# Performance work log

Measured on AMD Instinct MI355X. Metric: run time of the kernel, lower is better.

## Reference

```python
import jax, jax.numpy as jnp
import numpy as np

B, S, H, F, E, K = 2, 2048, 1024, 4096, 8, 2


def setup_inputs() -> dict:
    key = jax.random.key(0)
    ks = jax.random.split(key, 6)
    x = jax.random.normal(ks[0], (B, S, H), dtype=jnp.float32)
    probs = jax.random.uniform(ks[1], (K, B, S, 1), dtype=jnp.float32)
    experts = jax.random.randint(ks[2], (K, B, S, 1), 0, E, dtype=jnp.int32)
    # per-expert FFN params; 0.02 scale mimics typical transformer init
    w1 = jax.random.normal(ks[3], (E, H, F), dtype=jnp.float32) * 0.02
    b1 = jnp.zeros((E, F), dtype=jnp.float32)
    w2 = jax.random.normal(ks[4], (E, F, H), dtype=jnp.float32) * 0.02
    b2 = jnp.zeros((E, H), dtype=jnp.float32)
    return {"x": x, "probs": probs, "experts": experts,
            "w1": w1, "b1": b1, "w2": w2, "b2": b2}


def reference(x, probs, experts, w1, b1, w2, b2):
    # Dense compute-all-experts FFN: every expert processes every token.
    h = jnp.einsum('bsh,ehf->ebsf', x, w1) + b1[:, None, None, :]  # [E,B,S,F]
    h = jax.nn.gelu(h)
    y = jnp.einsum('ebsf,efh->ebsh', h, w2) + b2[:, None, None, :]  # [E,B,S,H]
    # Masked combine: sum_e sum_j probs_j * y_e * (experts_j == e)
    onehot = jax.nn.one_hot(experts[..., 0], w1.shape[0], dtype=x.dtype)  # [K,B,S,E]
    weights = jnp.einsum('kbsl,kbse->bse', probs, onehot)  # [B,S,E]
    out = jnp.einsum('bse,ebsh->bsh', weights, y)
    return out
```

## Files before the change

kernel.cpp:

```cpp
#include <hip/hip_runtime.h>
#include <stdint.h>

#define H_DIM 1024
#define F_DIM 4096
#define E_NUM 8
#define T_NUM 4096
#define NE    8192
#define BM    256
#define BN    256
#define BK    64
#define MAXT  40
#define PADM  9984
#define TBY   65536
#define LDSSZ (2*TBY)

#define G1_NWG (MAXT * (F_DIM / BN))
#define TRW2_NWG 4096

#define M_NT  0
#define M_PB  1
#define M_CNT 16
#define M_CUR 24
#define M_TE  32
#define M_TR  72
#define M_INTS 112

typedef float  f32x4  __attribute__((ext_vector_type(4)));
typedef short  bf16x8 __attribute__((ext_vector_type(8)));
typedef __bf16 b16v8  __attribute__((ext_vector_type(8)));
typedef unsigned short u16;
typedef u16    u16x8  __attribute__((ext_vector_type(8)));

#define BAR() __builtin_amdgcn_s_barrier()

__device__ __forceinline__ float gelu_tanh(float v) {
  float u = 0.7978845608028654f * (v + 0.044715f * v * v * v);
  return v / (1.0f + __expf(-2.0f * u));
}

__device__ __forceinline__ float b2f(u16 v) {
  union { float f; unsigned u; } x; x.u = ((unsigned)v) << 16; return x.f;
}

__device__ __forceinline__ void gl16(const void* g, void* l) {
  __builtin_amdgcn_global_load_lds(
      (const __attribute__((address_space(1))) unsigned int*)g,
      (__attribute__((address_space(3))) unsigned int*)l, 16, 0, 0);
}

__device__ __forceinline__ void trans_tile(const float* __restrict__ W, u16* __restrict__ Wt,
                                           int R, int C, int e, int bx, int by,
                                           char* L, int tid) {
  int r0 = by * 64, c0 = bx * 64;
  const float* We = W + (size_t)e * R * C;
  u16* Wte = Wt + (size_t)e * R * C;
#pragma unroll
  for (int it = 0; it < 4; ++it) {
    int gi = it * 256 + tid;
    int row = gi >> 4, c4 = gi & 15;
    f32x4 v = *(const f32x4*)(We + (size_t)(r0 + row) * C + c0 + c4 * 4);
    *(f32x4*)(L + row * 256 + ((c4 ^ (row & 15)) * 16)) = v;
  }
  __syncthreads();
#pragma unroll
  for (int s = 0; s < 2; ++s) {
    int chunk = s * 256 + tid;
    int c = chunk >> 3, rb = chunk & 7;
    b16v8 o;
#pragma unroll
    for (int j = 0; j < 8; ++j) {
      int r = rb * 8 + j;
      float f = *(const float*)(L + r * 256 + (((c >> 2) ^ (r & 15)) * 16) + (c & 3) * 4);
      o[j] = (__bf16)f;
    }
    *(b16v8*)(void*)(Wte + (size_t)(c0 + c) * R + r0 + rb * 8) = o;
  }
}


__global__ void k_init(int* tok, float* wgt, int* meta) {
  int i = blockIdx.x * 256 + threadIdx.x;
  if (i < PADM) { tok[i] = 0; wgt[i] = 0.f; }
  if (i < E_NUM) { meta[M_CNT + i] = 0; meta[M_CUR + i] = 0; }
}

__global__ void k_count(const int* __restrict__ experts, int* meta) {
  int i = blockIdx.x * 256 + threadIdx.x;
  int e = experts[i];
  int lane = threadIdx.x & 63;
#pragma unroll
  for (int ee = 0; ee < E_NUM; ++ee) {
    unsigned long long bm = __ballot(e == ee);
    if (e == ee && lane == __builtin_ctzll(bm))
      atomicAdd(&meta[M_CNT + ee], __popcll(bm));
  }
}

__global__ void k_plan(int* meta) {
  if (threadIdx.x != 0 || blockIdx.x != 0) return;
  int pb = 0, idx = 0;
  for (int e = 0; e < E_NUM; ++e) {
    int c = meta[M_CNT + e];
    int nt = (c + BM - 1) / BM;
    meta[M_PB + e] = pb;
    for (int t = 0; t < nt && idx < MAXT; ++t) {
      meta[M_TE + idx] = e; meta[M_TR + idx] = pb + t * BM; ++idx;
    }
    pb += nt * BM;
  }
  meta[M_NT] = idx;
}

__global__ void k_scatter(const int* __restrict__ experts, const float* __restrict__ probs,
                          int* tok, float* wgt, int* entpos, int* meta) {
  int i = blockIdx.x * 256 + threadIdx.x;
  int e = experts[i];
  int t = i & (T_NUM - 1);
  float p = probs[i];
  int lane = threadIdx.x & 63;
#pragma unroll
  for (int ee = 0; ee < E_NUM; ++ee) {
    unsigned long long bm = __ballot(e == ee);
    if (e == ee) {
      int leader = __builtin_ctzll(bm);
      int cnt = __popcll(bm);
      int base = 0;
      if (lane == leader) base = atomicAdd(&meta[M_CUR + ee], cnt);
      base = __shfl(base, leader);
      int rank = __popcll(bm & ((1ull << lane) - 1ull));
      int pos = meta[M_PB + ee] + base + rank;
      tok[pos] = t;
      wgt[pos] = p;
      entpos[i] = pos;
    }
  }
}

#define TRW1_NWG 4096
__global__ __launch_bounds__(512) void k_prep(const float* __restrict__ x, u16* __restrict__ xbf,
                                              const float* __restrict__ w1, u16* __restrict__ w1t) {
  int bid = blockIdx.x;
  if (bid < TRW1_NWG) {
    alignas(16) __shared__ char L[32768];
    int ti = bid * 2 + (threadIdx.x >> 8);
    int e = ti >> 10, rem = ti & 1023;
    int bx = rem & 63, by = rem >> 6;
    trans_tile(w1, w1t, H_DIM, F_DIM, e, bx, by, L + (threadIdx.x >> 8) * 16384, threadIdx.x & 255);
    return;
  }
  int i = (bid - TRW1_NWG) * 512 + threadIdx.x;
  const f32x4* xp = (const f32x4*)x;
  f32x4 a = xp[i * 2], b = xp[i * 2 + 1];
  b16v8 o;
  o[0] = (__bf16)a[0]; o[1] = (__bf16)a[1]; o[2] = (__bf16)a[2]; o[3] = (__bf16)a[3];
  o[4] = (__bf16)b[0]; o[5] = (__bf16)b[1]; o[6] = (__bf16)b[2]; o[7] = (__bf16)b[3];
  ((b16v8*)xbf)[i] = o;
}

__global__ __launch_bounds__(256) void k_trans(const float* __restrict__ W, u16* __restrict__ Wt,
                                               int R, int C) {
  alignas(16) __shared__ char L[16384];
  trans_tile(W, Wt, R, C, blockIdx.z, blockIdx.x, blockIdx.y, L, threadIdx.x);
}


#define STAGEALL(kt, sb)                                                      \
  { _Pragma("unroll")                                                         \
    for (int j = 0; j < 4; ++j)                                               \
      gl16(asrc[j] + (size_t)(kt) * BK, LDS + (sb) + j * 8192 + wid * 1024);  \
    _Pragma("unroll")                                                         \
    for (int j = 0; j < 4; ++j)                                               \
      gl16(bsrc[j] + (size_t)(kt) * BK, LDS + (sb) + 32768 + j * 8192 + wid * 1024); }

#define GEMM_COMPUTE(bb)                                                      \
  { const char* Ab_ = LDS + (bb); const char* Bb_ = LDS + (bb) + 32768;       \
    _Pragma("unroll")                                                         \
    for (int kk = 0; kk < 2; ++kk) {                                          \
      int kbyte = kk * 64 + ((lane >> 4) << 4);                               \
      bf16x8 af[8], bfr[4];                                                   \
      _Pragma("unroll")                                                       \
      for (int m = 0; m < 8; ++m) {                                           \
        int r = wr * 128 + m * 16 + (lane & 15);                              \
        af[m] = *(const bf16x8*)(Ab_ + r * 128 + (kbyte ^ ((r & 7) << 4)));   \
      }                                                                       \
      _Pragma("unroll")                                                       \
      for (int n = 0; n < 4; ++n) {                                           \
        int c = wc * 64 + n * 16 + (lane & 15);                               \
        bfr[n] = *(const bf16x8*)(Bb_ + c * 128 + (kbyte ^ ((c & 7) << 4)));  \
      }                                                                       \
      __builtin_amdgcn_s_setprio(1);                                          \
      _Pragma("unroll")                                                       \
      for (int m = 0; m < 8; ++m)                                             \
        _Pragma("unroll")                                                     \
        for (int n = 0; n < 4; ++n)                                           \
          acc[m][n] = __builtin_amdgcn_mfma_f32_16x16x32_bf16(af[m], bfr[n], acc[m][n], 0, 0, 0); \
      __builtin_amdgcn_s_setprio(0);                                          \
    } }

#define GEMM_KLOOP(NT)                                                        \
  STAGEALL(0, 0);                                                             \
  asm volatile("s_waitcnt vmcnt(0)" ::: "memory");                            \
  BAR();                                                                      \
  { int cur = 0;                                                              \
    for (int kt = 0; kt < (NT); ++kt) {                                       \
      if (kt + 1 < (NT)) STAGEALL(kt + 1, (cur ^ 1) * TBY);                   \
      GEMM_COMPUTE(cur * TBY);                                                \
      asm volatile("s_waitcnt vmcnt(0)" ::: "memory");                        \
      BAR();                                                                  \
      cur ^= 1;                                                               \
    } }


__global__ __launch_bounds__(512, 1) void k_gemm1(
    const u16* __restrict__ xbf, const u16* __restrict__ w1t, const float* __restrict__ b1,
    const int* __restrict__ tok, const int* __restrict__ meta, u16* __restrict__ hbuf,
    const float* __restrict__ w2, u16* __restrict__ w2t)
{
  extern __shared__ char LDS[];
  int wg = blockIdx.x;
  if (wg >= G1_NWG) {
    int ti = (wg - G1_NWG) * 2 + (threadIdx.x >> 8);
    int e = ti >> 10, rem = ti & 1023;
    int bx = rem & 15, by = rem >> 4;
    trans_tile(w2, w2t, F_DIM, H_DIM, e, bx, by, LDS + (threadIdx.x >> 8) * 16384, threadIdx.x & 255);
    return;
  }
  int work = (wg & 7) * (G1_NWG / 8) + (wg >> 3);
  int slot = work % MAXT;
  int cbase = (work / MAXT) * BN;
  int nt = meta[M_NT];
  if (slot >= nt) return;
  int e     = meta[M_TE + slot];
  int rbase = meta[M_TR + slot];

  int tid = threadIdx.x;
  int lane = tid & 63;
  int wid = tid >> 6;
  int wr = wid >> 2, wc = wid & 3;
  int cc = tid & 7, rr = tid >> 3;

  const u16* asrc[4]; const u16* bsrc[4];
#pragma unroll
  for (int j = 0; j < 4; ++j) {
    int rj = j * 64 + rr;
    int t = tok[rbase + rj];
    asrc[j] = xbf + (size_t)t * H_DIM + ((cc ^ (rj & 7)) * 8);
    bsrc[j] = w1t + ((size_t)e * F_DIM + cbase + rj) * H_DIM + ((cc ^ (rj & 7)) * 8);
  }

  f32x4 acc[8][4];
#pragma unroll
  for (int m = 0; m < 8; ++m)
#pragma unroll
    for (int n = 0; n < 4; ++n) acc[m][n] = (f32x4){0.f, 0.f, 0.f, 0.f};

  GEMM_KLOOP(H_DIM / BK)

  float bv[4];
#pragma unroll
  for (int n = 0; n < 4; ++n) bv[n] = b1[e * F_DIM + cbase + wc * 64 + n * 16 + (lane & 15)];
  char* reg = LDS + wid * 16384;
#pragma unroll
  for (int m = 0; m < 8; ++m)
#pragma unroll
    for (int n = 0; n < 4; ++n)
#pragma unroll
      for (int q = 0; q < 4; ++q) {
        float v = acc[m][n][q] + bv[n];
        v = gelu_tanh(v);
        int row4 = ((lane >> 4) << 2) + q;
        int col = n * 16 + (lane & 15);
        *(__bf16*)(reg + m * 2048 + row4 * 128 + col * 2) = (__bf16)v;
      }
#pragma unroll
  for (int q = 0; q < 16; ++q) {
    int m = q >> 1, p = q & 1;
    int byte = p * 1024 + lane * 16;
    u16x8 v = *(const u16x8*)(reg + m * 2048 + byte);
    int row  = p * 8 + (lane >> 3);
    int colb = (lane & 7) * 16;
    size_t grow = (size_t)(rbase + wr * 128 + m * 16 + row);
    size_t gcol = (size_t)(cbase + wc * 64 + (colb >> 1));
    *(u16x8*)(hbuf + grow * F_DIM + gcol) = v;
  }
}


__global__ __launch_bounds__(512, 1) void k_gemm2(
    const u16* __restrict__ hbuf, const u16* __restrict__ w2t, const float* __restrict__ b2,
    const int* __restrict__ meta, u16* __restrict__ ybuf)
{
  extern __shared__ char LDS[];
  int wg = blockIdx.x;
  int work = (wg & 7) * 40 + (wg >> 3);
  int zi   = work / 160;
  int rem  = work % 160;
  int slot = rem % MAXT;
  int cbase = (rem / MAXT) * BN;
  int kzb   = zi * (F_DIM / 2);
  int nt = meta[M_NT];
  if (slot >= nt) return;
  int e     = meta[M_TE + slot];
  int rbase = meta[M_TR + slot];

  int tid = threadIdx.x;
  int lane = tid & 63;
  int wid = tid >> 6;
  int wr = wid >> 2, wc = wid & 3;
  int cc = tid & 7, rr = tid >> 3;

  const u16* asrc[4]; const u16* bsrc[4];
#pragma unroll
  for (int j = 0; j < 4; ++j) {
    int rj = j * 64 + rr;
    asrc[j] = hbuf + (size_t)(rbase + rj) * F_DIM + kzb + ((cc ^ (rj & 7)) * 8);
    bsrc[j] = w2t + ((size_t)e * H_DIM + cbase + rj) * F_DIM + kzb + ((cc ^ (rj & 7)) * 8);
  }

  f32x4 acc[8][4];
#pragma unroll
  for (int m = 0; m < 8; ++m)
#pragma unroll
    for (int n = 0; n < 4; ++n) acc[m][n] = (f32x4){0.f, 0.f, 0.f, 0.f};

  GEMM_KLOOP((F_DIM / 2) / BK)

  bool z0 = (zi == 0);
  u16* yb = ybuf + (size_t)zi * PADM * H_DIM;
  float bv[4];
#pragma unroll
  for (int n = 0; n < 4; ++n)
    bv[n] = z0 ? b2[e * H_DIM + cbase + wc * 64 + n * 16 + (lane & 15)] : 0.f;
  char* reg = LDS + wid * 16384;
#pragma unroll
  for (int m = 0; m < 8; ++m)
#pragma unroll
    for (int n = 0; n < 4; ++n)
#pragma unroll
      for (int q = 0; q < 4; ++q) {
        float v = acc[m][n][q] + bv[n];
        int row4 = ((lane >> 4) << 2) + q;
        int col = n * 16 + (lane & 15);
        *(__bf16*)(reg + m * 2048 + row4 * 128 + col * 2) = (__bf16)v;
      }
#pragma unroll
  for (int q = 0; q < 16; ++q) {
    int m = q >> 1, p = q & 1;
    int byte = p * 1024 + lane * 16;
    u16x8 v = *(const u16x8*)(reg + m * 2048 + byte);
    int row  = p * 8 + (lane >> 3);
    int colb = (lane & 7) * 16;
    size_t grow = (size_t)(rbase + wr * 128 + m * 16 + row);
    size_t gcol = (size_t)(cbase + wc * 64 + (colb >> 1));
    *(u16x8*)(yb + grow * H_DIM + gcol) = v;
  }
}


__global__ __launch_bounds__(256) void k_combine(
    const u16* __restrict__ ybuf, const float* __restrict__ wgt,
    const int* __restrict__ entpos, float* __restrict__ out)
{
  int idx = blockIdx.x * 256 + threadIdx.x;
  int t = idx >> 7, hc = idx & 127;
  int p0 = entpos[t], p1 = entpos[T_NUM + t];
  float w0 = wgt[p0], w1 = wgt[p1];
  const u16x8* y0 = (const u16x8*)(ybuf);
  const u16x8* y1 = (const u16x8*)(ybuf + (size_t)PADM * H_DIM);
  u16x8 a = y0[(size_t)p0 * (H_DIM / 8) + hc];
  u16x8 b = y1[(size_t)p0 * (H_DIM / 8) + hc];
  u16x8 c = y0[(size_t)p1 * (H_DIM / 8) + hc];
  u16x8 d = y1[(size_t)p1 * (H_DIM / 8) + hc];
  f32x4 o0, o1;
#pragma unroll
  for (int j = 0; j < 4; ++j)
    o0[j] = w0 * (b2f(a[j]) + b2f(b[j])) + w1 * (b2f(c[j]) + b2f(d[j]));
#pragma unroll
  for (int j = 0; j < 4; ++j)
    o1[j] = w0 * (b2f(a[4 + j]) + b2f(b[4 + j])) + w1 * (b2f(c[4 + j]) + b2f(d[4 + j]));
  f32x4* op = (f32x4*)(out + (size_t)t * H_DIM + hc * 8);
  op[0] = o0;
  op[1] = o1;
}


extern "C" void kernel_launch(void* const* d_in, const int* in_sizes, int n_in,
                              void* d_out, int out_size, void* d_ws, size_t ws_size,
                              hipStream_t stream)
{
  const float* x       = (const float*)d_in[0];
  const float* probs   = (const float*)d_in[1];
  const int*   experts = (const int*)d_in[2];
  const float* w1      = (const float*)d_in[3];
  const float* b1      = (const float*)d_in[4];
  const float* w2      = (const float*)d_in[5];
  const float* b2      = (const float*)d_in[6];
  float* out = (float*)d_out;

  char* ws = (char*)d_ws;
  size_t off = 0;
  u16*   hbuf = (u16*)(ws + off);  off += (size_t)PADM * F_DIM * sizeof(u16);
  u16*   xbf  = (u16*)(ws + off);  off += (size_t)T_NUM * H_DIM * sizeof(u16);
  u16*   w1t  = (u16*)(ws + off);  off += (size_t)E_NUM * F_DIM * H_DIM * sizeof(u16);
  u16*   ybuf = (u16*)(ws + off);  off += (size_t)2 * PADM * H_DIM * sizeof(u16);
  int*   tok  = (int*)(ws + off);  off += (size_t)PADM * sizeof(int);
  float* wgt  = (float*)(ws + off); off += (size_t)PADM * sizeof(float);
  int*   entpos = (int*)(ws + off); off += (size_t)NE * sizeof(int);
  int*   meta = (int*)(ws + off);  off += M_INTS * sizeof(int);
  size_t w2t_bytes = (size_t)E_NUM * F_DIM * H_DIM * sizeof(u16);
  bool fused = (ws_size >= off + w2t_bytes);
  u16* w2t = fused ? (u16*)(ws + off) : w1t;
  (void)in_sizes; (void)n_in;

  hipFuncSetAttribute(reinterpret_cast<const void*>(&k_gemm1),
                      hipFuncAttributeMaxDynamicSharedMemorySize, LDSSZ);
  hipFuncSetAttribute(reinterpret_cast<const void*>(&k_gemm2),
                      hipFuncAttributeMaxDynamicSharedMemorySize, LDSSZ);

  k_init   <<<dim3((PADM + 255) / 256), 256, 0, stream>>>(tok, wgt, meta);
  k_count  <<<dim3(NE / 256), 256, 0, stream>>>(experts, meta);
  k_plan   <<<1, 1, 0, stream>>>(meta);
  k_scatter<<<dim3(NE / 256), 256, 0, stream>>>(experts, probs, tok, wgt, entpos, meta);
  k_prep   <<<dim3(TRW1_NWG + T_NUM * H_DIM / 8 / 512), 512, 0, stream>>>(x, xbf, w1, w1t);
  k_gemm1  <<<dim3(G1_NWG + (fused ? TRW2_NWG : 0)), 512, LDSSZ, stream>>>(
              xbf, w1t, b1, tok, meta, hbuf, w2, w2t);
  if (!fused)
    k_trans<<<dim3(H_DIM / 64, F_DIM / 64, E_NUM), 256, 0, stream>>>(w2, w2t, F_DIM, H_DIM);
  k_gemm2  <<<dim3(MAXT * (H_DIM / BN) * 2), 512, LDSSZ, stream>>>(hbuf, w2t, b2, meta, ybuf);
  k_combine<<<dim3(T_NUM * H_DIM / 8 / 256), 256, 0, stream>>>(ybuf, wgt, entpos, out);
}
```

Baseline: 341.4 us.

## Use persistent grid-stride GEMM2 with four-way split-K reusing w1t workspace

```diff
diff --git a/kernel.cpp b/kernel.cpp
--- a/kernel.cpp
+++ b/kernel.cpp
@@ -16,6 +16,7 @@
 
 #define G1_NWG (MAXT * (F_DIM / BN))
 #define TRW2_NWG 4096
+#define TRW1_NWG 4096
 
 #define M_NT  0
 #define M_PB  1
@@ -136,7 +137,6 @@
   }
 }
 
-#define TRW1_NWG 4096
 __global__ __launch_bounds__(512) void k_prep(const float* __restrict__ x, u16* __restrict__ xbf,
                                               const float* __restrict__ w1, u16* __restrict__ w1t) {
   int bid = blockIdx.x;
@@ -286,22 +286,17 @@
 }
 
 
+template<int ZS, int GRID>
 __global__ __launch_bounds__(512, 1) void k_gemm2(
     const u16* __restrict__ hbuf, const u16* __restrict__ w2t, const float* __restrict__ b2,
     const int* __restrict__ meta, u16* __restrict__ ybuf)
 {
   extern __shared__ char LDS[];
+  const int NIT = MAXT * 4 * ZS;
+  const int KT  = (F_DIM / ZS) / BK;
   int wg = blockIdx.x;
-  int work = (wg & 7) * 40 + (wg >> 3);
-  int zi   = work / 160;
-  int rem  = work % 160;
-  int slot = rem % MAXT;
-  int cbase = (rem / MAXT) * BN;
-  int kzb   = zi * (F_DIM / 2);
+  int work0 = (wg & 7) * (GRID / 8) + (wg >> 3);
   int nt = meta[M_NT];
-  if (slot >= nt) return;
-  int e     = meta[M_TE + slot];
-  int rbase = meta[M_TR + slot];
 
   int tid = threadIdx.x;
   int lane = tid & 63;
@@ -309,54 +304,69 @@
   int wr = wid >> 2, wc = wid & 3;
   int cc = tid & 7, rr = tid >> 3;
 
-  const u16* asrc[4]; const u16* bsrc[4];
-#pragma unroll
-  for (int j = 0; j < 4; ++j) {
-    int rj = j * 64 + rr;
-    asrc[j] = hbuf + (size_t)(rbase + rj) * F_DIM + kzb + ((cc ^ (rj & 7)) * 8);
-    bsrc[j] = w2t + ((size_t)e * H_DIM + cbase + rj) * F_DIM + kzb + ((cc ^ (rj & 7)) * 8);
-  }
-
-  f32x4 acc[8][4];
-#pragma unroll
-  for (int m = 0; m < 8; ++m)
-#pragma unroll
-    for (int n = 0; n < 4; ++n) acc[m][n] = (f32x4){0.f, 0.f, 0.f, 0.f};
-
-  GEMM_KLOOP((F_DIM / 2) / BK)
-
-  bool z0 = (zi == 0);
-  u16* yb = ybuf + (size_t)zi * PADM * H_DIM;
-  float bv[4];
-#pragma unroll
-  for (int n = 0; n < 4; ++n)
-    bv[n] = z0 ? b2[e * H_DIM + cbase + wc * 64 + n * 16 + (lane & 15)] : 0.f;
-  char* reg = LDS + wid * 16384;
-#pragma unroll
-  for (int m = 0; m < 8; ++m)
+  for (int item = work0; item < NIT; item += GRID) {
+    int slot = item / (4 * ZS);
+    int rem  = item % (4 * ZS);
+    int cb   = rem / ZS;
+    int zi   = rem % ZS;
+    if (slot >= nt) continue;
+    int e     = meta[M_TE + slot];
+    int rbase = meta[M_TR + slot];
+    int cbase = cb * BN;
+    int kzb   = zi * (F_DIM / ZS);
+
+    __syncthreads();
+
+    const u16* asrc[4]; const u16* bsrc[4];
+#pragma unroll
+    for (int j = 0; j < 4; ++j) {
+      int rj = j * 64 + rr;
+      asrc[j] = hbuf + (size_t)(rbase + rj) * F_DIM + kzb + ((cc ^ (rj & 7)) * 8);
+      bsrc[j] = w2t + ((size_t)e * H_DIM + cbase + rj) * F_DIM + kzb + ((cc ^ (rj & 7)) * 8);
+    }
+
+    f32x4 acc[8][4];
+#pragma unroll
+    for (int m = 0; m < 8; ++m)
+#pragma unroll
+      for (int n = 0; n < 4; ++n) acc[m][n] = (f32x4){0.f, 0.f, 0.f, 0.f};
+
+    GEMM_KLOOP(KT)
+
+    bool z0 = (zi == 0);
+    u16* yb = ybuf + (size_t)zi * PADM * H_DIM;
+    float bv[4];
 #pragma unroll
     for (int n = 0; n < 4; ++n)
-#pragma unroll
-      for (int q = 0; q < 4; ++q) {
-        float v = acc[m][n][q] + bv[n];
-        int row4 = ((lane >> 4) << 2) + q;
-        int col = n * 16 + (lane & 15);
-        *(__bf16*)(reg + m * 2048 + row4 * 128 + col * 2) = (__bf16)v;
-      }
-#pragma unroll
-  for (int q = 0; q < 16; ++q) {
-    int m = q >> 1, p = q & 1;
-    int byte = p * 1024 + lane * 16;
-    u16x8 v = *(const u16x8*)(reg + m * 2048 + byte);
-    int row  = p * 8 + (lane >> 3);
-    int colb = (lane & 7) * 16;
-    size_t grow = (size_t)(rbase + wr * 128 + m * 16 + row);
-    size_t gcol = (size_t)(cbase + wc * 64 + (colb >> 1));
-    *(u16x8*)(yb + grow * H_DIM + gcol) = v;
-  }
-}
-
-
+      bv[n] = z0 ? b2[e * H_DIM + cbase + wc * 64 + n * 16 + (lane & 15)] : 0.f;
+    char* reg = LDS + wid * 16384;
+#pragma unroll
+    for (int m = 0; m < 8; ++m)
+#pragma unroll
+      for (int n = 0; n < 4; ++n)
+#pragma unroll
+        for (int q = 0; q < 4; ++q) {
+          float v = acc[m][n][q] + bv[n];
+          int row4 = ((lane >> 4) << 2) + q;
+          int col = n * 16 + (lane & 15);
+          *(__bf16*)(reg + m * 2048 + row4 * 128 + col * 2) = (__bf16)v;
+        }
+#pragma unroll
+    for (int q = 0; q < 16; ++q) {
+      int m = q >> 1, p = q & 1;
+      int byte = p * 1024 + lane * 16;
+      u16x8 v = *(const u16x8*)(reg + m * 2048 + byte);
+      int row  = p * 8 + (lane >> 3);
+      int colb = (lane & 7) * 16;
+      size_t grow = (size_t)(rbase + wr * 128 + m * 16 + row);
+      size_t gcol = (size_t)(cbase + wc * 64 + (colb >> 1));
+      *(u16x8*)(yb + grow * H_DIM + gcol) = v;
+    }
+  }
+}
+
+
+template<int ZS>
 __global__ __launch_bounds__(256) void k_combine(
     const u16* __restrict__ ybuf, const float* __restrict__ wgt,
     const int* __restrict__ entpos, float* __restrict__ out)
@@ -365,19 +375,22 @@
   int t = idx >> 7, hc = idx & 127;
   int p0 = entpos[t], p1 = entpos[T_NUM + t];
   float w0 = wgt[p0], w1 = wgt[p1];
-  const u16x8* y0 = (const u16x8*)(ybuf);
-  const u16x8* y1 = (const u16x8*)(ybuf + (size_t)PADM * H_DIM);
-  u16x8 a = y0[(size_t)p0 * (H_DIM / 8) + hc];
-  u16x8 b = y1[(size_t)p0 * (H_DIM / 8) + hc];
-  u16x8 c = y0[(size_t)p1 * (H_DIM / 8) + hc];
-  u16x8 d = y1[(size_t)p1 * (H_DIM / 8) + hc];
+  float s0[8], s1[8];
+#pragma unroll
+  for (int j = 0; j < 8; ++j) { s0[j] = 0.f; s1[j] = 0.f; }
+#pragma unroll
+  for (int z = 0; z < ZS; ++z) {
+    const u16x8* yz = (const u16x8*)(ybuf + (size_t)z * PADM * H_DIM);
+    u16x8 a = yz[(size_t)p0 * (H_DIM / 8) + hc];
+    u16x8 b = yz[(size_t)p1 * (H_DIM / 8) + hc];
+#pragma unroll
+    for (int j = 0; j < 8; ++j) { s0[j] += b2f(a[j]); s1[j] += b2f(b[j]); }
+  }
   f32x4 o0, o1;
 #pragma unroll
-  for (int j = 0; j < 4; ++j)
-    o0[j] = w0 * (b2f(a[j]) + b2f(b[j])) + w1 * (b2f(c[j]) + b2f(d[j]));
-#pragma unroll
-  for (int j = 0; j < 4; ++j)
-    o1[j] = w0 * (b2f(a[4 + j]) + b2f(b[4 + j])) + w1 * (b2f(c[4 + j]) + b2f(d[4 + j]));
+  for (int j = 0; j < 4; ++j) o0[j] = w0 * s0[j] + w1 * s1[j];
+#pragma unroll
+  for (int j = 0; j < 4; ++j) o1[j] = w0 * s0[4 + j] + w1 * s1[4 + j];
   f32x4* op = (f32x4*)(out + (size_t)t * H_DIM + hc * 8);
   op[0] = o0;
   op[1] = o1;
@@ -410,11 +423,14 @@
   size_t w2t_bytes = (size_t)E_NUM * F_DIM * H_DIM * sizeof(u16);
   bool fused = (ws_size >= off + w2t_bytes);
   u16* w2t = fused ? (u16*)(ws + off) : w1t;
+  u16* ybuf4 = w1t;
   (void)in_sizes; (void)n_in;
 
   hipFuncSetAttribute(reinterpret_cast<const void*>(&k_gemm1),
                       hipFuncAttributeMaxDynamicSharedMemorySize, LDSSZ);
-  hipFuncSetAttribute(reinterpret_cast<const void*>(&k_gemm2),
+  hipFuncSetAttribute(reinterpret_cast<const void*>(&k_gemm2<4, 512>),
+                      hipFuncAttributeMaxDynamicSharedMemorySize, LDSSZ);
+  hipFuncSetAttribute(reinterpret_cast<const void*>(&k_gemm2<2, 320>),
                       hipFuncAttributeMaxDynamicSharedMemorySize, LDSSZ);
 
   k_init   <<<dim3((PADM + 255) / 256), 256, 0, stream>>>(tok, wgt, meta);
@@ -424,8 +440,12 @@
   k_prep   <<<dim3(TRW1_NWG + T_NUM * H_DIM / 8 / 512), 512, 0, stream>>>(x, xbf, w1, w1t);
   k_gemm1  <<<dim3(G1_NWG + (fused ? TRW2_NWG : 0)), 512, LDSSZ, stream>>>(
               xbf, w1t, b1, tok, meta, hbuf, w2, w2t);
-  if (!fused)
+  if (fused) {
+    k_gemm2<4, 512><<<dim3(512), 512, LDSSZ, stream>>>(hbuf, w2t, b2, meta, ybuf4);
+    k_combine<4><<<dim3(T_NUM * H_DIM / 8 / 256), 256, 0, stream>>>(ybuf4, wgt, entpos, out);
+  } else {
     k_trans<<<dim3(H_DIM / 64, F_DIM / 64, E_NUM), 256, 0, stream>>>(w2, w2t, F_DIM, H_DIM);
-  k_gemm2  <<<dim3(MAXT * (H_DIM / BN) * 2), 512, LDSSZ, stream>>>(hbuf, w2t, b2, meta, ybuf);
-  k_combine<<<dim3(T_NUM * H_DIM / 8 / 256), 256, 0, stream>>>(ybuf, wgt, entpos, out);
-}
+    k_gemm2<2, 320><<<dim3(320), 512, LDSSZ, stream>>>(hbuf, w2t, b2, meta, ybuf);
+    k_combine<2><<<dim3(T_NUM * H_DIM / 8 / 256), 256, 0, stream>>>(ybuf, wgt, entpos, out);
+  }
+}
```

New measurement: 369.8 us. +8.3%, slower.

## Restructure GEMM k-loop into 8-phase schedule interleaving LDS reads, global stages, MFMAs

Applied to the files above, without the earlier changes.

```diff
diff --git a/kernel.cpp b/kernel.cpp
--- a/kernel.cpp
+++ b/kernel.cpp
@@ -16,6 +16,7 @@
 
 #define G1_NWG (MAXT * (F_DIM / BN))
 #define TRW2_NWG 4096
+#define TRW1_NWG 4096
 
 #define M_NT  0
 #define M_PB  1
@@ -31,7 +32,9 @@
 typedef unsigned short u16;
 typedef u16    u16x8  __attribute__((ext_vector_type(8)));
 
-#define BAR() __builtin_amdgcn_s_barrier()
+#define BAR()   __builtin_amdgcn_s_barrier()
+#define FENCE() asm volatile("" ::: "memory")
+#define LGKM0() asm volatile("s_waitcnt lgkmcnt(0)" ::: "memory")
 
 __device__ __forceinline__ float gelu_tanh(float v) {
   float u = 0.7978845608028654f * (v + 0.044715f * v * v * v);
@@ -136,7 +139,6 @@
   }
 }
 
-#define TRW1_NWG 4096
 __global__ __launch_bounds__(512) void k_prep(const float* __restrict__ x, u16* __restrict__ xbf,
                                               const float* __restrict__ w1, u16* __restrict__ w1t) {
   int bid = blockIdx.x;
@@ -164,48 +166,70 @@
 }
 
 
-#define STAGEALL(kt, sb)                                                      \
-  { _Pragma("unroll")                                                         \
-    for (int j = 0; j < 4; ++j)                                               \
-      gl16(asrc[j] + (size_t)(kt) * BK, LDS + (sb) + j * 8192 + wid * 1024);  \
-    _Pragma("unroll")                                                         \
-    for (int j = 0; j < 4; ++j)                                               \
-      gl16(bsrc[j] + (size_t)(kt) * BK, LDS + (sb) + 32768 + j * 8192 + wid * 1024); }
-
-#define GEMM_COMPUTE(bb)                                                      \
-  { const char* Ab_ = LDS + (bb); const char* Bb_ = LDS + (bb) + 32768;       \
-    _Pragma("unroll")                                                         \
-    for (int kk = 0; kk < 2; ++kk) {                                          \
-      int kbyte = kk * 64 + ((lane >> 4) << 4);                               \
-      bf16x8 af[8], bfr[4];                                                   \
-      _Pragma("unroll")                                                       \
-      for (int m = 0; m < 8; ++m) {                                           \
-        int r = wr * 128 + m * 16 + (lane & 15);                              \
-        af[m] = *(const bf16x8*)(Ab_ + r * 128 + (kbyte ^ ((r & 7) << 4)));   \
-      }                                                                       \
-      _Pragma("unroll")                                                       \
-      for (int n = 0; n < 4; ++n) {                                           \
-        int c = wc * 64 + n * 16 + (lane & 15);                               \
-        bfr[n] = *(const bf16x8*)(Bb_ + c * 128 + (kbyte ^ ((c & 7) << 4)));  \
-      }                                                                       \
-      __builtin_amdgcn_s_setprio(1);                                          \
-      _Pragma("unroll")                                                       \
-      for (int m = 0; m < 8; ++m)                                             \
-        _Pragma("unroll")                                                     \
-        for (int n = 0; n < 4; ++n)                                           \
-          acc[m][n] = __builtin_amdgcn_mfma_f32_16x16x32_bf16(af[m], bfr[n], acc[m][n], 0, 0, 0); \
-      __builtin_amdgcn_s_setprio(0);                                          \
-    } }
-
-#define GEMM_KLOOP(NT)                                                        \
-  STAGEALL(0, 0);                                                             \
-  asm volatile("s_waitcnt vmcnt(0)" ::: "memory");                            \
+#define STG_A(kt, dbb, h)                                                     \
+  { gl16(asrc[2*(h)]   + (size_t)(kt) * BK, LDS + (dbb) + (2*(h))   * 8192 + wid * 1024); \
+    gl16(asrc[2*(h)+1] + (size_t)(kt) * BK, LDS + (dbb) + (2*(h)+1) * 8192 + wid * 1024); }
+#define STG_B(kt, dbb, h)                                                     \
+  { gl16(bsrc[2*(h)]   + (size_t)(kt) * BK, LDS + (dbb) + 32768 + (2*(h))   * 8192 + wid * 1024); \
+    gl16(bsrc[2*(h)+1] + (size_t)(kt) * BK, LDS + (dbb) + 32768 + (2*(h)+1) * 8192 + wid * 1024); }
+
+#define LD_A(dst, mi, kk)                                                     \
+  { int r_ = wr * 128 + (mi) * 16 + (lane & 15);                              \
+    int kb_ = (kk) * 64 + ((lane >> 4) << 4);                                 \
+    dst = *(const bf16x8*)(Ab_ + r_ * 128 + (kb_ ^ ((r_ & 7) << 4))); }
+#define LD_B(dst, ni, kk)                                                     \
+  { int c_ = wc * 64 + (ni) * 16 + (lane & 15);                               \
+    int kb_ = (kk) * 64 + ((lane >> 4) << 4);                                 \
+    dst = *(const bf16x8*)(Bb_ + c_ * 128 + (kb_ ^ ((c_ & 7) << 4))); }
+
+#define MFMA16(p)                                                             \
+  __builtin_amdgcn_s_setprio(1);                                              \
+  _Pragma("unroll") for (int mm = 0; mm < 2; ++mm)                            \
+    _Pragma("unroll") for (int n = 0; n < 4; ++n) {                           \
+      acc[2*(p)+mm][n] = __builtin_amdgcn_mfma_f32_16x16x32_bf16(af[mm][0], bfr[n][0], acc[2*(p)+mm][n], 0, 0, 0); \
+      acc[2*(p)+mm][n] = __builtin_amdgcn_mfma_f32_16x16x32_bf16(af[mm][1], bfr[n][1], acc[2*(p)+mm][n], 0, 0, 0); \
+    }                                                                         \
+  __builtin_amdgcn_s_setprio(0);
+
+#define GEMM_KLOOP_8P(NT)                                                     \
+  STG_A(0, 0, 0); STG_A(0, 0, 1); STG_B(0, 0, 0); STG_B(0, 0, 1);             \
+  STG_B(1, TBY, 0); STG_B(1, TBY, 1);                                         \
+  asm volatile("s_waitcnt vmcnt(4)" ::: "memory");                            \
   BAR();                                                                      \
   { int cur = 0;                                                              \
     for (int kt = 0; kt < (NT); ++kt) {                                       \
-      if (kt + 1 < (NT)) STAGEALL(kt + 1, (cur ^ 1) * TBY);                   \
-      GEMM_COMPUTE(cur * TBY);                                                \
-      asm volatile("s_waitcnt vmcnt(0)" ::: "memory");                        \
+      const int db = cur * TBY, dn = (cur ^ 1) * TBY;                         \
+      const char* Ab_ = LDS + db;                                             \
+      const char* Bb_ = LDS + db + 32768;                                     \
+      bf16x8 bfr[4][2], af[2][2];                                             \
+                                                                 \
+      FENCE();                                                                \
+      _Pragma("unroll") for (int n = 0; n < 4; ++n) { LD_B(bfr[n][0], n, 0); LD_B(bfr[n][1], n, 1); } \
+      LD_A(af[0][0], 0, 0); LD_A(af[0][1], 0, 1); LD_A(af[1][0], 1, 0); LD_A(af[1][1], 1, 1); \
+      if (kt + 1 < (NT)) STG_A(kt + 1, dn, 0);                                \
+      FENCE(); BAR(); LGKM0();                                                \
+      MFMA16(0);                                                              \
+      FENCE(); BAR();                                                         \
+                                                                 \
+      LD_A(af[0][0], 2, 0); LD_A(af[0][1], 2, 1); LD_A(af[1][0], 3, 0); LD_A(af[1][1], 3, 1); \
+      if (kt + 1 < (NT)) STG_A(kt + 1, dn, 1);                                \
+      FENCE(); BAR(); LGKM0();                                                \
+      MFMA16(1);                                                              \
+      FENCE(); BAR();                                                         \
+                                                                 \
+      LD_A(af[0][0], 4, 0); LD_A(af[0][1], 4, 1); LD_A(af[1][0], 5, 0); LD_A(af[1][1], 5, 1); \
+      if (kt + 2 < (NT)) STG_B(kt + 2, db, 0);                                \
+      FENCE(); BAR(); LGKM0();                                                \
+      MFMA16(2);                                                              \
+      FENCE(); BAR();                                                         \
+                                                                 \
+      LD_A(af[0][0], 6, 0); LD_A(af[0][1], 6, 1); LD_A(af[1][0], 7, 0); LD_A(af[1][1], 7, 1); \
+      if (kt + 2 < (NT)) STG_B(kt + 2, db, 1);                                \
+      FENCE(); BAR(); LGKM0();                                                \
+      MFMA16(3);                                                              \
+      FENCE();                                                                \
+      if (kt == (NT) - 2)     { asm volatile("s_waitcnt vmcnt(0)" ::: "memory"); } \
+      else if (kt < (NT) - 2) { asm volatile("s_waitcnt vmcnt(4)" ::: "memory"); } \
       BAR();                                                                  \
       cur ^= 1;                                                               \
     } }
@@ -254,7 +278,7 @@
 #pragma unroll
     for (int n = 0; n < 4; ++n) acc[m][n] = (f32x4){0.f, 0.f, 0.f, 0.f};
 
-  GEMM_KLOOP(H_DIM / BK)
+  GEMM_KLOOP_8P(H_DIM / BK)
 
   float bv[4];
 #pragma unroll
@@ -323,7 +347,7 @@
 #pragma unroll
     for (int n = 0; n < 4; ++n) acc[m][n] = (f32x4){0.f, 0.f, 0.f, 0.f};
 
-  GEMM_KLOOP((F_DIM / 2) / BK)
+  GEMM_KLOOP_8P((F_DIM / 2) / BK)
 
   bool z0 = (zi == 0);
   u16* yb = ybuf + (size_t)zi * PADM * H_DIM;
```

New measurement: 331.0 us. 3.0% less time.
